# Optimization experiments

Measured on AMD Instinct MI355X. Metric: run time of the kernel, lower is better.

Reference implementation:

```python
import jax, jax.numpy as jnp
import numpy as np

DIM = 1024
NUM_HEADS = 16
HEAD_DIM = DIM // NUM_HEADS
N_PREFIX = 5
SCALE = HEAD_DIM ** -0.5


def _rotate_half(x):
    h = x.shape[-1] // 2
    return jnp.concatenate([-x[..., h:], x[..., :h]], axis=-1)


def _apply_rope(x, cos, sin):
    return x * cos + _rotate_half(x) * sin


def setup_inputs() -> dict:
    key = jax.random.key(0)
    ks = jax.random.split(key, 12)
    B, S = 8, N_PREFIX + 1024
    x = jax.random.normal(ks[0], (B, S, DIM), dtype=jnp.float32)
    rope_cos = jax.random.uniform(ks[1], (1024, HEAD_DIM), dtype=jnp.float32)
    rope_sin = jax.random.uniform(ks[2], (1024, HEAD_DIM), dtype=jnp.float32)
    sd = DIM ** -0.5
    Wq = jax.random.normal(ks[3], (DIM, DIM), dtype=jnp.float32) * sd
    bq = jnp.zeros((DIM,), dtype=jnp.float32)
    Wk = jax.random.normal(ks[4], (DIM, DIM), dtype=jnp.float32) * sd
    Wv = jax.random.normal(ks[5], (DIM, DIM), dtype=jnp.float32) * sd
    bv = jnp.zeros((DIM,), dtype=jnp.float32)
    Wo = jax.random.normal(ks[6], (DIM, DIM), dtype=jnp.float32) * sd
    bo = jnp.zeros((DIM,), dtype=jnp.float32)
    return {"x": x, "rope_cos": rope_cos, "rope_sin": rope_sin,
            "Wq": Wq, "bq": bq, "Wk": Wk, "Wv": Wv, "bv": bv,
            "Wo": Wo, "bo": bo}


def reference(x, rope_cos, rope_sin, Wq, bq, Wk, Wv, bv, Wo, bo):
    B, S, D = x.shape
    # projections: Q and V have bias, K has no bias
    q = (x @ Wq + bq).reshape(B, S, NUM_HEADS, HEAD_DIM).transpose(0, 2, 1, 3)
    k = (x @ Wk).reshape(B, S, NUM_HEADS, HEAD_DIM).transpose(0, 2, 1, 3)
    v = (x @ Wv + bv).reshape(B, S, NUM_HEADS, HEAD_DIM).transpose(0, 2, 1, 3)
    # 2D RoPE on patch tokens only (prefix tokens untouched)
    cos = rope_cos[None, None]  # [1,1,P,hd]
    sin = rope_sin[None, None]
    q = jnp.concatenate([q[:, :, :N_PREFIX], _apply_rope(q[:, :, N_PREFIX:], cos, sin)], axis=2)
    k = jnp.concatenate([k[:, :, :N_PREFIX], _apply_rope(k[:, :, N_PREFIX:], cos, sin)], axis=2)
    q = q * SCALE
    attn = jax.nn.softmax(jnp.einsum('bhqd,bhkd->bhqk', q, k), axis=-1)
    out = jnp.einsum('bhqk,bhkd->bhqd', attn, v)
    out = out.transpose(0, 2, 1, 3).reshape(B, S, D)
    return out @ Wo + bo
```

## Files before the change

kernel.cpp:

```cpp
#include <hip/hip_runtime.h>

typedef unsigned short u16;
typedef __bf16 bf16x8 __attribute__((ext_vector_type(8)));
typedef unsigned short u16x8 __attribute__((ext_vector_type(8)));
typedef float f32x4 __attribute__((ext_vector_type(4)));

#define M_ROWS 8232
#define SEQ 1029
#define NPREF 5
#define DIMN 1024
#define NH 16
#define HD 64

#define BAR_LGKM asm volatile("s_waitcnt lgkmcnt(0)\ns_barrier" ::: "memory")

typedef __attribute__((address_space(1))) const unsigned char as1_u8;
typedef __attribute__((address_space(3))) unsigned char as3_u8;

__device__ __forceinline__ void gload_lds16(const u16* g, u16* l) {
  __builtin_amdgcn_global_load_lds((as1_u8*)g, (as3_u8*)l, 16, 0, 0);
}

__device__ __forceinline__ u16 f2bf(float f) {
  unsigned u = __float_as_uint(f);
  u += 0x7fffu + ((u >> 16) & 1u);
  return (u16)(u >> 16);
}

__device__ __forceinline__ unsigned pk2bf(float lo, float hi) {
  unsigned ul = __float_as_uint(lo);
  unsigned uh = __float_as_uint(hi);
  ul += 0x7fffu + ((ul >> 16) & 1u);
  uh += 0x7fffu + ((uh >> 16) & 1u);
  return __builtin_amdgcn_perm(uh, ul, 0x07060302u);
}

__global__ __launch_bounds__(256) void k_pack_x(const float* __restrict__ x, u16* __restrict__ Xp) {
  int cb = blockIdx.x;
  int rb = blockIdx.y;
  __shared__ u16 Tl[64 * 264];
  int t = threadIdx.x;
#pragma unroll
  for (int p = 0; p < 16; ++p) {
    int idx = p * 256 + t;
    int row = idx >> 6;
    int c4 = idx & 63;
    int grow = rb * 64 + row; if (grow >= M_ROWS) grow = M_ROWS - 1;
    float4 v = *reinterpret_cast<const float4*>(x + (size_t)grow * DIMN + cb * 256 + c4 * 4);
    ushort4 o;
    o.x = f2bf(v.x); o.y = f2bf(v.y); o.z = f2bf(v.z); o.w = f2bf(v.w);
    *reinterpret_cast<ushort4*>(&Tl[row * 264 + c4 * 4]) = o;
  }
  __syncthreads();
  int wv = t >> 6, lane = t & 63;
  int mt = rb >> 1, g = rb & 1;
#pragma unroll
  for (int li = 0; li < 8; ++li) {
    int ll = wv * 8 + li;
    int i = ll >> 3;
    int kkl = ll & 7;
    int row = i * 16 + (lane & 15);
    int col = kkl * 32 + (lane >> 4) * 8;
    uint4 d = *reinterpret_cast<const uint4*>(&Tl[row * 264 + col]);
    size_t line = ((size_t)(mt * 2 + g) * 4 + i) * 32 + (cb * 8 + kkl);
    *reinterpret_cast<uint4*>(Xp + line * 512 + lane * 8) = d;
  }
}

__global__ __launch_bounds__(256) void k_wt(const float* __restrict__ W0, const float* __restrict__ W1,
                                            const float* __restrict__ W2, const float* __restrict__ W3,
                                            u16* __restrict__ P0, u16* __restrict__ P1,
                                            u16* __restrict__ P2, u16* __restrict__ P3) {
  const float* W; u16* P;
  switch (blockIdx.z) {
    case 0: W = W0; P = P0; break;
    case 1: W = W1; P = P1; break;
    case 2: W = W2; P = P2; break;
    default: W = W3; P = P3; break;
  }
  __shared__ float tile[64 * 68];
  int t = threadIdx.x;
  int kb = blockIdx.x, nb = blockIdx.y;
#pragma unroll
  for (int p = 0; p < 16; ++p) {
    int idx = p * 256 + t;
    int row = idx >> 6, col = idx & 63;
    tile[row * 68 + col] = W[(size_t)(kb * 64 + row) * DIMN + nb * 64 + col];
  }
  __syncthreads();
  int wv = t >> 6, lane = t & 63;
#pragma unroll
  for (int li = 0; li < 2; ++li) {
    int ll = wv * 2 + li;
    int jg = ll >> 1, kkl = ll & 1;
    int n = jg * 16 + (lane & 15);
    int kc = kkl * 32 + (lane >> 4) * 8;
    u16 buf[8];
#pragma unroll
    for (int dk = 0; dk < 8; ++dk) buf[dk] = f2bf(tile[(kc + dk) * 68 + n]);
    size_t line = (size_t)(nb * 4 + jg) * 32 + kb * 2 + kkl;
    *reinterpret_cast<uint4*>(P + line * 512 + lane * 8) = *reinterpret_cast<const uint4*>(buf);
  }
}

#define MM16(AF, BF) do { \
  _Pragma("unroll") for (int i_ = 0; i_ < 4; ++i_) \
  _Pragma("unroll") for (int j_ = 0; j_ < 4; ++j_) \
    acc[i_][j_] = __builtin_amdgcn_mfma_f32_16x16x32_bf16(AF[i_], BF[j_], acc[i_][j_], 0, 0, 0); \
} while (0)

__global__ __launch_bounds__(256) void k_qkv(
    const u16* __restrict__ Xp,
    const u16* __restrict__ Pq, const u16* __restrict__ Pk, const u16* __restrict__ Pv,
    const float* __restrict__ bq, const float* __restrict__ bv,
    const float* __restrict__ rc, const float* __restrict__ rs,
    u16* __restrict__ Qg, u16* __restrict__ Kg, u16* __restrict__ Vg)
{
  int bid = blockIdx.x;
  int xcd = bid & 7;
  int s = bid >> 3;
  int nt = s & 7;
  int s2 = s >> 3;
  int mode = s2 / 9;
  int mtq = s2 - mode * 9;
  int mt = mtq * 8 + xcd;
  if (mt >= 65) return;
  const u16* Wp = (mode == 0) ? Pq : (mode == 1) ? Pk : Pv;
  u16* dst = (mode == 0) ? Qg : (mode == 1) ? Kg : Vg;
  int m0 = mt * 128, n0 = nt * 128;

  int t = threadIdx.x, lane = t & 63, wv = t >> 6;
  int fr = lane & 15, quad = lane >> 4;
  int ga = wv >> 1, gb = wv & 1;
  int wm = ga * 64, wn = gb * 64;

  __shared__ u16 S[16][512];

  const u16* gsrc[4];
  u16* ldst[4];
#pragma unroll
  for (int q = 0; q < 4; ++q) {
    int ls = wv * 4 + q;
    const u16* base;
    int lineIdx;
    if (ls < 8) {
      int g = ls >> 2, i = ls & 3;
      base = Xp; lineIdx = ((mt * 2 + g) * 4 + i) * 32;
    } else {
      int l2 = ls - 8;
      int g = l2 >> 2, j = l2 & 3;
      base = Wp; lineIdx = ((nt * 2 + g) * 4 + j) * 32;
    }
    gsrc[q] = base + (size_t)lineIdx * 512 + lane * 8;
    ldst[q] = &S[ls][0];
  }

  const u16* ards[4];
  const u16* brds[4];
#pragma unroll
  for (int i = 0; i < 4; ++i) {
    ards[i] = &S[ga * 4 + i][lane * 8];
    brds[i] = &S[8 + gb * 4 + i][lane * 8];
  }

  f32x4 zero4 = {0.f, 0.f, 0.f, 0.f};
  f32x4 acc[4][4];
#pragma unroll
  for (int i = 0; i < 4; ++i)
#pragma unroll
    for (int j = 0; j < 4; ++j) acc[i][j] = zero4;

  for (int kk = 0; kk < 32; ++kk) {
#pragma unroll
    for (int q = 0; q < 4; ++q)
      gload_lds16(gsrc[q] + (size_t)kk * 512, ldst[q]);
    __syncthreads();
    bf16x8 a[4], b[4];
#pragma unroll
    for (int i = 0; i < 4; ++i) {
      a[i] = *reinterpret_cast<const bf16x8*>(ards[i]);
      b[i] = *reinterpret_cast<const bf16x8*>(brds[i]);
    }
    MM16(a, b);
    __syncthreads();
  }

  int h = (n0 + wn) >> 6;
#pragma unroll
  for (int i = 0; i < 4; ++i) {
    int rowbase = m0 + wm + i * 16 + quad * 4;
#pragma unroll
    for (int r = 0; r < 4; ++r) {
      int row = rowbase + r;
      if (row >= M_ROWS) continue;
      int b = row / SEQ;
      int sI = row - b * SEQ;
#pragma unroll
      for (int j = 0; j < 4; ++j) {
        int d = j * 16 + fr;
        float v = acc[i][j][r];
        float outv;
        if (mode == 2) {
          outv = v + bv[n0 + wn + d];
        } else {
          float vb = v;
          int jp = j ^ 2;
          float pv = acc[i][jp][r];
          if (mode == 0) {
            vb += bq[n0 + wn + d];
            pv += bq[n0 + wn + (jp * 16 + fr)];
          }
          if (sI >= NPREF) {
            int p = sI - NPREF;
            float c = rc[p * HD + d];
            float sn = rs[p * HD + d];
            float rot = (d < 32) ? -pv : pv;
            outv = vb * c + rot * sn;
          } else {
            outv = vb;
          }
          if (mode == 0) outv *= 0.125f;
        }
        dst[((size_t)(b * NH + h) * SEQ + sI) * HD + d] = f2bf(outv);
      }
    }
  }
}

__global__ __launch_bounds__(256) void k_attn(
    const u16* __restrict__ Qg, const u16* __restrict__ Kg, const u16* __restrict__ Vg,
    u16* __restrict__ AOp)
{
  int bh = blockIdx.x;
  int mtb = blockIdx.y;
  int q0 = mtb * 128;
  int b = bh >> 4, h = bh & 15;
  const size_t base = (size_t)bh * SEQ * HD;

  __shared__ u16 KV[128 * 72];
  __shared__ u16 Ps[4][32 * 72];
  u16* Ks = KV;
  u16* Vt = KV + 64 * 72;

  int t = threadIdx.x, lane = t & 63, wv = t >> 6;
  int fr = lane & 15, quad = lane >> 4;

  int ki = t >> 2;
  int kc0 = (t & 3) * 16;
  int vs0 = (t & 31) * 2;
  int vdo = (t >> 5) * 8;

  bf16x8 qf[2][2];
#pragma unroll
  for (int qt = 0; qt < 2; ++qt) {
#pragma unroll
    for (int st = 0; st < 2; ++st) {
      int row = q0 + wv * 32 + qt * 16 + fr;
      if (row >= SEQ) row = SEQ - 1;
      qf[qt][st] = *reinterpret_cast<const bf16x8*>(Qg + base + (size_t)row * HD + st * 32 + quad * 8);
    }
  }

  u16x8 one16 = {0x3F80, 0x3F80, 0x3F80, 0x3F80, 0x3F80, 0x3F80, 0x3F80, 0x3F80};
  bf16x8 vone = __builtin_bit_cast(bf16x8, one16);

  f32x4 zero4 = {0.f, 0.f, 0.f, 0.f};
  f32x4 o[2][5];
#pragma unroll
  for (int qt = 0; qt < 2; ++qt)
#pragma unroll
    for (int di = 0; di < 5; ++di) o[qt][di] = zero4;

  uint4 krA0, krA1, vrA0, vrA1;
  {
    int kr = ki; if (kr >= SEQ) kr = SEQ - 1;
    const u16* ksrc = Kg + base + (size_t)kr * HD;
    krA0 = *reinterpret_cast<const uint4*>(ksrc + kc0);
    krA1 = *reinterpret_cast<const uint4*>(ksrc + kc0 + 8);
    int r0 = vs0; if (r0 >= SEQ) r0 = SEQ - 1;
    int r1 = vs0 + 1; if (r1 >= SEQ) r1 = SEQ - 1;
    vrA0 = *reinterpret_cast<const uint4*>(Vg + base + (size_t)r0 * HD + vdo);
    vrA1 = *reinterpret_cast<const uint4*>(Vg + base + (size_t)r1 * HD + vdo);
  }

  for (int kt = 0; kt < 17; ++kt) {
    int k0 = kt * 64;
    BAR_LGKM;
    *reinterpret_cast<uint4*>(&Ks[ki * 72 + kc0]) = krA0;
    *reinterpret_cast<uint4*>(&Ks[ki * 72 + kc0 + 8]) = krA1;
    {
      u16 v0[8], v1[8];
      *reinterpret_cast<uint4*>(v0) = vrA0;
      *reinterpret_cast<uint4*>(v1) = vrA1;
#pragma unroll
      for (int j = 0; j < 8; ++j) {
        unsigned pk = (unsigned)v0[j] | ((unsigned)v1[j] << 16);
        *reinterpret_cast<unsigned*>(&Vt[(vdo + j) * 72 + vs0]) = pk;
      }
    }
    if (kt < 16) {
      int kn = k0 + 64;
      int kr = kn + ki; if (kr >= SEQ) kr = SEQ - 1;
      const u16* ksrc = Kg + base + (size_t)kr * HD;
      krA0 = *reinterpret_cast<const uint4*>(ksrc + kc0);
      krA1 = *reinterpret_cast<const uint4*>(ksrc + kc0 + 8);
      int r0 = kn + vs0; if (r0 >= SEQ) r0 = SEQ - 1;
      int r1 = kn + vs0 + 1; if (r1 >= SEQ) r1 = SEQ - 1;
      vrA0 = *reinterpret_cast<const uint4*>(Vg + base + (size_t)r0 * HD + vdo);
      vrA1 = *reinterpret_cast<const uint4*>(Vg + base + (size_t)r1 * HD + vdo);
    }
    BAR_LGKM;

    f32x4 sc[4][2];
#pragma unroll
    for (int mi = 0; mi < 4; ++mi)
#pragma unroll
      for (int qt = 0; qt < 2; ++qt) sc[mi][qt] = zero4;
#pragma unroll
    for (int st = 0; st < 2; ++st) {
#pragma unroll
      for (int mi = 0; mi < 4; ++mi) {
        bf16x8 kf = *reinterpret_cast<const bf16x8*>(&Ks[(mi * 16 + fr) * 72 + st * 32 + quad * 8]);
#pragma unroll
        for (int qt = 0; qt < 2; ++qt)
          sc[mi][qt] = __builtin_amdgcn_mfma_f32_16x16x32_bf16(kf, qf[qt][st], sc[mi][qt], 0, 0, 0);
      }
    }

    bool last = (kt == 16);
#pragma unroll
    for (int qt = 0; qt < 2; ++qt) {
#pragma unroll
      for (int mi = 0; mi < 4; ++mi) {
        float p0, p1, p2, p3;
        {
          float s0v = sc[mi][qt][0], s1v = sc[mi][qt][1], s2v = sc[mi][qt][2], s3v = sc[mi][qt][3];
          if (last) {
            int kc = mi * 16 + quad * 4;
            if (kc + 0 >= NPREF) s0v = -1e30f;
            if (kc + 1 >= NPREF) s1v = -1e30f;
            if (kc + 2 >= NPREF) s2v = -1e30f;
            if (kc + 3 >= NPREF) s3v = -1e30f;
          }
          p0 = __expf(s0v - 16.0f);
          p1 = __expf(s1v - 16.0f);
          p2 = __expf(s2v - 16.0f);
          p3 = __expf(s3v - 16.0f);
        }
        unsigned d0 = pk2bf(p0, p1);
        unsigned d1 = pk2bf(p2, p3);
        uint2 w; w.x = d0; w.y = d1;
        *reinterpret_cast<uint2*>(&Ps[wv][(qt * 16 + fr) * 72 + mi * 16 + quad * 4]) = w;
      }
    }

#pragma unroll
    for (int st = 0; st < 2; ++st) {
      bf16x8 pf[2];
#pragma unroll
      for (int qt = 0; qt < 2; ++qt)
        pf[qt] = *reinterpret_cast<const bf16x8*>(&Ps[wv][(qt * 16 + fr) * 72 + st * 32 + quad * 8]);
#pragma unroll
      for (int di = 0; di < 4; ++di) {
        bf16x8 vf = *reinterpret_cast<const bf16x8*>(&Vt[(di * 16 + fr) * 72 + st * 32 + quad * 8]);
#pragma unroll
        for (int qt = 0; qt < 2; ++qt)
          o[qt][di] = __builtin_amdgcn_mfma_f32_16x16x32_bf16(pf[qt], vf, o[qt][di], 0, 0, 0);
      }
#pragma unroll
      for (int qt = 0; qt < 2; ++qt)
        o[qt][4] = __builtin_amdgcn_mfma_f32_16x16x32_bf16(pf[qt], vone, o[qt][4], 0, 0, 0);
    }
  }

  __syncthreads();
#pragma unroll
  for (int qt = 0; qt < 2; ++qt) {
#pragma unroll
    for (int r = 0; r < 4; ++r) {
      int rowl = wv * 32 + qt * 16 + quad * 4 + r;
      bool valid = (q0 + rowl) < SEQ;
      float inv = valid ? (1.f / o[qt][4][r]) : 0.f;
#pragma unroll
      for (int di = 0; di < 4; ++di)
        KV[rowl * 72 + di * 16 + fr] = f2bf(o[qt][di][r] * inv);
    }
  }
  __syncthreads();
#pragma unroll
  for (int li = 0; li < 4; ++li) {
    int ll = wv * 4 + li;
    int g = ll >> 3, i = (ll >> 1) & 3, kkl = ll & 1;
    int rowl = g * 64 + i * 16 + (lane & 15);
    int col = kkl * 32 + (lane >> 4) * 8;
    uint4 d = *reinterpret_cast<const uint4*>(&KV[rowl * 72 + col]);
    size_t line = ((size_t)((b * 9 + mtb) * 2 + g) * 4 + i) * 32 + (h * 2 + kkl);
    *reinterpret_cast<uint4*>(AOp + line * 512 + lane * 8) = d;
  }
}

__global__ __launch_bounds__(256) void k_out(
    const u16* __restrict__ AOp, const u16* __restrict__ Po,
    const float* __restrict__ bo, float* __restrict__ Out)
{
  int bid = blockIdx.x;
  int xcd = bid & 7;
  int s = bid >> 3;
  int nt = s & 7;
  int mtq = s >> 3;
  int mid = mtq * 8 + xcd;
  int b = mid / 9, mtb = mid - b * 9;
  int n0 = nt * 128;

  int t = threadIdx.x, lane = t & 63, wv = t >> 6;
  int fr = lane & 15, quad = lane >> 4;
  int ga = wv >> 1, gb = wv & 1;
  int wm = ga * 64, wn = gb * 64;

  __shared__ u16 S[16][512];

  const u16* gsrc[4];
  u16* ldst[4];
#pragma unroll
  for (int q = 0; q < 4; ++q) {
    int ls = wv * 4 + q;
    const u16* base;
    int lineIdx;
    if (ls < 8) {
      int g = ls >> 2, i = ls & 3;
      base = AOp; lineIdx = ((mid * 2 + g) * 4 + i) * 32;
    } else {
      int l2 = ls - 8;
      int g = l2 >> 2, j = l2 & 3;
      base = Po; lineIdx = ((nt * 2 + g) * 4 + j) * 32;
    }
    gsrc[q] = base + (size_t)lineIdx * 512 + lane * 8;
    ldst[q] = &S[ls][0];
  }

  const u16* ards[4];
  const u16* brds[4];
#pragma unroll
  for (int i = 0; i < 4; ++i) {
    ards[i] = &S[ga * 4 + i][lane * 8];
    brds[i] = &S[8 + gb * 4 + i][lane * 8];
  }

  f32x4 zero4 = {0.f, 0.f, 0.f, 0.f};
  f32x4 acc[4][4];
#pragma unroll
  for (int i = 0; i < 4; ++i)
#pragma unroll
    for (int j = 0; j < 4; ++j) acc[i][j] = zero4;

  for (int kk = 0; kk < 32; ++kk) {
#pragma unroll
    for (int q = 0; q < 4; ++q)
      gload_lds16(gsrc[q] + (size_t)kk * 512, ldst[q]);
    __syncthreads();
    bf16x8 a[4], b2[4];
#pragma unroll
    for (int i = 0; i < 4; ++i) {
      a[i] = *reinterpret_cast<const bf16x8*>(ards[i]);
      b2[i] = *reinterpret_cast<const bf16x8*>(brds[i]);
    }
    MM16(a, b2);
    __syncthreads();
  }

#pragma unroll
  for (int i = 0; i < 4; ++i) {
    int rowbase = mtb * 128 + wm + i * 16 + quad * 4;
#pragma unroll
    for (int r = 0; r < 4; ++r) {
      int rowl = rowbase + r;
      if (rowl >= SEQ) continue;
      size_t row = (size_t)b * SEQ + rowl;
#pragma unroll
      for (int j = 0; j < 4; ++j) {
        int col = n0 + wn + j * 16 + fr;
        Out[row * DIMN + col] = acc[i][j][r] + bo[col];
      }
    }
  }
}

extern "C" void kernel_launch(void* const* d_in, const int* in_sizes, int n_in,
                              void* d_out, int out_size, void* d_ws, size_t ws_size,
                              hipStream_t stream)
{
  const float* x  = (const float*)d_in[0];
  const float* rc = (const float*)d_in[1];
  const float* rs = (const float*)d_in[2];
  const float* Wq = (const float*)d_in[3];
  const float* bq = (const float*)d_in[4];
  const float* Wk = (const float*)d_in[5];
  const float* Wv = (const float*)d_in[6];
  const float* bv = (const float*)d_in[7];
  const float* Wo = (const float*)d_in[8];
  const float* bo = (const float*)d_in[9];
  float* Out = (float*)d_out;

  u16* p = (u16*)d_ws;
  u16* Xp = p; p += (size_t)16640 * 512;
  u16* Pq = p; p += (size_t)2048 * 512;
  u16* Pk = p; p += (size_t)2048 * 512;
  u16* Pv = p; p += (size_t)2048 * 512;
  u16* Po = p; p += (size_t)2048 * 512;
  u16* Qg = p; p += (size_t)M_ROWS * DIMN;
  u16* Kg = p; p += (size_t)M_ROWS * DIMN;
  u16* Vg = p; p += (size_t)M_ROWS * DIMN;
  u16* AOp = Xp;

  dim3 gx(4, 130);
  k_pack_x<<<gx, 256, 0, stream>>>(x, Xp);
  dim3 gt(16, 16, 4);
  k_wt<<<gt, 256, 0, stream>>>(Wq, Wk, Wv, Wo, Pq, Pk, Pv, Po);
  k_qkv<<<1728, 256, 0, stream>>>(Xp, Pq, Pk, Pv, bq, bv, rc, rs, Qg, Kg, Vg);
  dim3 g2(128, 9);
  k_attn<<<g2, 256, 0, stream>>>(Qg, Kg, Vg, AOp);
  k_out<<<576, 256, 0, stream>>>(AOp, Po, bo, Out);
}
```

Measured before the change: 336.6 us.

## Triple-buffer LDS tiles with async prefetch in QKV and output GEMMs

Replaces the single-buffered K loop in the QKV and output projection GEMMs with a three-stage LDS ring. Global-to-LDS loads are issued two iterations ahead, and partial vmcnt waits let the MFMA work on the current tile overlap the loads for later tiles. The cost is three times the LDS per block (48 KB), which may reduce occupancy. Correctness now depends on the hand-coded vmcnt counts and raw barriers.

```diff
diff --git a/kernel.cpp b/kernel.cpp
--- a/kernel.cpp
+++ b/kernel.cpp
@@ -107,6 +107,41 @@
   _Pragma("unroll") for (int i_ = 0; i_ < 4; ++i_) \
   _Pragma("unroll") for (int j_ = 0; j_ < 4; ++j_) \
     acc[i_][j_] = __builtin_amdgcn_mfma_f32_16x16x32_bf16(AF[i_], BF[j_], acc[i_][j_], 0, 0, 0); \
+} while (0)
+
+#define STAGE(bufI, tt) do { \
+  _Pragma("unroll") for (int q_ = 0; q_ < 4; ++q_) \
+    gload_lds16(gsrc[q_] + (size_t)(tt) * 512, Sb + (bufI) * 8192 + (wv * 4 + q_) * 512); \
+} while (0)
+
+#define KLOOP32 do { \
+  STAGE(0, 0); \
+  STAGE(1, 1); \
+  int cur = 0, stg = 2; \
+  for (int kk = 0; kk < 32; ++kk) { \
+    if (kk + 2 < 32) { \
+      STAGE(stg, kk + 2); \
+      asm volatile("s_waitcnt vmcnt(8)" ::: "memory"); \
+    } else if (kk + 1 < 32) { \
+      asm volatile("s_waitcnt vmcnt(4)" ::: "memory"); \
+    } else { \
+      asm volatile("s_waitcnt vmcnt(0)" ::: "memory"); \
+    } \
+    __builtin_amdgcn_s_barrier(); \
+    asm volatile("" ::: "memory"); \
+    const u16* rd_ = Sb + cur * 8192; \
+    bf16x8 a_[4], bfr_[4]; \
+    _Pragma("unroll") for (int i_ = 0; i_ < 4; ++i_) { \
+      a_[i_]   = *reinterpret_cast<const bf16x8*>(rd_ + (ga * 4 + i_) * 512 + lane * 8); \
+      bfr_[i_] = *reinterpret_cast<const bf16x8*>(rd_ + (8 + gb * 4 + i_) * 512 + lane * 8); \
+    } \
+    MM16(a_, bfr_); \
+    asm volatile("" ::: "memory"); \
+    __builtin_amdgcn_s_barrier(); \
+    cur = cur + 1; if (cur == 3) cur = 0; \
+    stg = stg + 1; if (stg == 3) stg = 0; \
+  } \
+  asm volatile("s_waitcnt vmcnt(0)" ::: "memory"); \
 } while (0)
 
 __global__ __launch_bounds__(256) void k_qkv(
@@ -134,10 +169,10 @@
   int ga = wv >> 1, gb = wv & 1;
   int wm = ga * 64, wn = gb * 64;
 
-  __shared__ u16 S[16][512];
+  __shared__ u16 S[3 * 16 * 512];
+  u16* Sb = S;
 
   const u16* gsrc[4];
-  u16* ldst[4];
 #pragma unroll
   for (int q = 0; q < 4; ++q) {
     int ls = wv * 4 + q;
@@ -152,15 +187,6 @@
       base = Wp; lineIdx = ((nt * 2 + g) * 4 + j) * 32;
     }
     gsrc[q] = base + (size_t)lineIdx * 512 + lane * 8;
-    ldst[q] = &S[ls][0];
-  }
-
-  const u16* ards[4];
-  const u16* brds[4];
-#pragma unroll
-  for (int i = 0; i < 4; ++i) {
-    ards[i] = &S[ga * 4 + i][lane * 8];
-    brds[i] = &S[8 + gb * 4 + i][lane * 8];
   }
 
   f32x4 zero4 = {0.f, 0.f, 0.f, 0.f};
@@ -170,20 +196,7 @@
 #pragma unroll
     for (int j = 0; j < 4; ++j) acc[i][j] = zero4;
 
-  for (int kk = 0; kk < 32; ++kk) {
-#pragma unroll
-    for (int q = 0; q < 4; ++q)
-      gload_lds16(gsrc[q] + (size_t)kk * 512, ldst[q]);
-    __syncthreads();
-    bf16x8 a[4], b[4];
-#pragma unroll
-    for (int i = 0; i < 4; ++i) {
-      a[i] = *reinterpret_cast<const bf16x8*>(ards[i]);
-      b[i] = *reinterpret_cast<const bf16x8*>(brds[i]);
-    }
-    MM16(a, b);
-    __syncthreads();
-  }
+  KLOOP32;
 
   int h = (n0 + wn) >> 6;
 #pragma unroll
@@ -417,10 +430,10 @@
   int ga = wv >> 1, gb = wv & 1;
   int wm = ga * 64, wn = gb * 64;
 
-  __shared__ u16 S[16][512];
+  __shared__ u16 S[3 * 16 * 512];
+  u16* Sb = S;
 
   const u16* gsrc[4];
-  u16* ldst[4];
 #pragma unroll
   for (int q = 0; q < 4; ++q) {
     int ls = wv * 4 + q;
@@ -435,15 +448,6 @@
       base = Po; lineIdx = ((nt * 2 + g) * 4 + j) * 32;
     }
     gsrc[q] = base + (size_t)lineIdx * 512 + lane * 8;
-    ldst[q] = &S[ls][0];
-  }
-
-  const u16* ards[4];
-  const u16* brds[4];
-#pragma unroll
-  for (int i = 0; i < 4; ++i) {
-    ards[i] = &S[ga * 4 + i][lane * 8];
-    brds[i] = &S[8 + gb * 4 + i][lane * 8];
   }
 
   f32x4 zero4 = {0.f, 0.f, 0.f, 0.f};
@@ -453,20 +457,7 @@
 #pragma unroll
     for (int j = 0; j < 4; ++j) acc[i][j] = zero4;
 
-  for (int kk = 0; kk < 32; ++kk) {
-#pragma unroll
-    for (int q = 0; q < 4; ++q)
-      gload_lds16(gsrc[q] + (size_t)kk * 512, ldst[q]);
-    __syncthreads();
-    bf16x8 a[4], b2[4];
-#pragma unroll
-    for (int i = 0; i < 4; ++i) {
-      a[i] = *reinterpret_cast<const bf16x8*>(ards[i]);
-      b2[i] = *reinterpret_cast<const bf16x8*>(brds[i]);
-    }
-    MM16(a, b2);
-    __syncthreads();
-  }
+  KLOOP32;
 
 #pragma unroll
   for (int i = 0; i < 4; ++i) {
```

Result: faster. 313.7 us (-6.8%).
